# Performance work log

Hardware: AMD Instinct MI355X
Metric: run time of the kernel (lower is better)

Reference implementation:

```python
import jax, jax.numpy as jnp
import numpy as np

MODEL_DIM = 1024
NUM_HEADS = 16
HEAD_DIM = MODEL_DIM // NUM_HEADS
B, L = 2, 2048


def setup_inputs() -> dict:
    key = jax.random.key(0)
    ks = jax.random.split(key, 11)
    s = 1.0 / np.sqrt(MODEL_DIM)
    inp = {
        "q": jax.random.normal(ks[0], (B, L, MODEL_DIM), jnp.float32),
        "k": jax.random.normal(ks[1], (B, L, MODEL_DIM), jnp.float32),
        "v": jax.random.normal(ks[2], (B, L, MODEL_DIM), jnp.float32),
        "Wq": jax.random.uniform(ks[3], (MODEL_DIM, MODEL_DIM), jnp.float32, -s, s),
        "bq": jax.random.uniform(ks[4], (MODEL_DIM,), jnp.float32, -s, s),
        "Wk": jax.random.uniform(ks[5], (MODEL_DIM, MODEL_DIM), jnp.float32, -s, s),
        "bk": jax.random.uniform(ks[6], (MODEL_DIM,), jnp.float32, -s, s),
        "Wv": jax.random.uniform(ks[7], (MODEL_DIM, MODEL_DIM), jnp.float32, -s, s),
        "bv": jax.random.uniform(ks[8], (MODEL_DIM,), jnp.float32, -s, s),
        "Wo": jax.random.uniform(ks[9], (MODEL_DIM, MODEL_DIM), jnp.float32, -s, s),
        "bo": jax.random.uniform(ks[10], (MODEL_DIM,), jnp.float32, -s, s),
    }
    return inp


def reference(q, k, v, Wq, bq, Wk, bk, Wv, bv, Wo, bo):
    Bq, Lq, D = q.shape
    H, Hd = NUM_HEADS, HEAD_DIM
    # Linear projections (torch Linear: x @ W.T + b)
    Q = q @ Wq.T + bq
    K = k @ Wk.T + bk
    V = v @ Wv.T + bv
    # split heads -> [B, H, L, Hd]
    def split(x):
        return x.reshape(Bq, Lq, H, Hd).transpose(0, 2, 1, 3)
    Qh, Kh, Vh = split(Q), split(K), split(V)
    scale = 1.0 / jnp.sqrt(jnp.asarray(Hd, Q.dtype))
    scores = jnp.einsum("bhqd,bhkd->bhqk", Qh, Kh) * scale
    attn = jax.nn.softmax(scores, axis=-1)  # dropout = identity in eval
    ctx = jnp.einsum("bhqk,bhkd->bhqd", attn, Vh)
    ctx = ctx.transpose(0, 2, 1, 3).reshape(Bq, Lq, D)
    return ctx @ Wo.T + bo
```

## Files before the change

kernel.cpp:

```cpp
#include <hip/hip_runtime.h>


typedef __attribute__((ext_vector_type(4))) float f32x4;
typedef __attribute__((ext_vector_type(16))) float f32x16;
typedef __attribute__((ext_vector_type(4))) unsigned int u32x4;
typedef __attribute__((ext_vector_type(2))) unsigned int u32x2;
typedef __attribute__((ext_vector_type(8))) short bf16x8;

#define DEVI static __device__ __forceinline__

DEVI unsigned short f2bf(float x) {
  union { float f; unsigned u; } v; v.f = x;
  unsigned r = v.u + 0x7fffu + ((v.u >> 16) & 1u);
  return (unsigned short)(r >> 16);
}

DEVI unsigned cvtpk(float lo, float hi) {
  unsigned r;
  asm("v_cvt_pk_bf16_f32 %0, %1, %2" : "=v"(r) : "v"(lo), "v"(hi));
  return r;
}

DEVI float exp2v(float x) {
  float y;
  asm("v_exp_f32 %0, %1" : "=v"(y) : "v"(x));
  return y;
}

DEVI void gload_lds16(const void* g, void* l) {
  __builtin_amdgcn_global_load_lds((__attribute__((address_space(1))) void*)g,
                                   (__attribute__((address_space(3))) void*)l, 16, 0, 0);
}

#define WAIT_VM(N) asm volatile("s_waitcnt vmcnt(" #N ")" ::: "memory")
#define BARRIER __builtin_amdgcn_s_barrier()

constexpr int MD = 1024;
constexpr int NH = 16;
constexpr int HD = 64;
constexpr int LL = 2048;
constexpr float CQ = 0.18033688011112042f;

struct Cvt4Args { const float* src[4]; unsigned short* dst[4]; };

__global__ void cvt4_kernel(Cvt4Args a) {
  const int which = blockIdx.x >> 9;
  const int i = ((blockIdx.x & 511) * 256 + threadIdx.x) * 8;
  const float* w = a.src[which];
  unsigned short* o = a.dst[which];
  f32x4 x = *(const f32x4*)(w + i);
  f32x4 y = *(const f32x4*)(w + i + 4);
  union { unsigned u[4]; u32x4 q; } r;
  r.u[0] = cvtpk(x[0], x[1]); r.u[1] = cvtpk(x[2], x[3]);
  r.u[2] = cvtpk(y[0], y[1]); r.u[3] = cvtpk(y[2], y[3]);
  *(u32x4*)(o + i) = r.q;
}

struct QKVArgs {
  const float* A[3];
  const unsigned short* W[3];
  const float* bias[3];
  unsigned short* out[3];
};

__global__ __launch_bounds__(256, 2) void gemm_qkv(QKVArgs args) {
  __shared__ alignas(16) float Afl[2][128 * 32];
  __shared__ alignas(16) unsigned short Bl[2][128 * 32];

  const int tid = threadIdx.x;
  const int lane = tid & 63;
  const int wave = tid >> 6;
  const int wr = wave >> 1, wc = wave & 1;
  const int lr = lane & 15, lg = lane >> 4;

  const int logical = (int)(blockIdx.x & 7) * 96 + (int)(blockIdx.x >> 3);
  const int n0 = (logical & 7) * 128;
  const int y = logical >> 3;
  const int mode = y >> 5;
  const int m0 = (y & 31) * 128;

  const float* Af = args.A[mode];
  const unsigned short* Wb = args.W[mode];
  const float* bias = args.bias[mode];
  unsigned short* Out = args.out[mode];

  const int arow_l = lane >> 3, aslot = lane & 7;
  const int wrow_l = lane >> 2, wslot = lane & 3;

  f32x4 acc[4][4] = {};

  auto stage = [&](int b, int kt) {
    const int k0 = kt * 32;
    #pragma unroll
    for (int sh = 0; sh < 4; ++sh) {
      const int row = sh * 32 + wave * 8 + arow_l;
      const int ss = aslot ^ (row & 7);
      gload_lds16((const char*)(Af + (size_t)(m0 + row) * 1024 + k0) + ss * 16,
                  (char*)&Afl[b][0] + sh * 4096 + wave * 1024);
    }
    #pragma unroll
    for (int sh = 0; sh < 2; ++sh) {
      const int row = sh * 64 + wave * 16 + wrow_l;
      const int ss = wslot ^ ((row >> 1) & 3);
      gload_lds16((const char*)(Wb + (size_t)(n0 + row) * 1024 + k0) + ss * 16,
                  (char*)&Bl[b][0] + sh * 4096 + wave * 1024);
    }
  };

  stage(0, 0);

  for (int kt = 0; kt < 32; ++kt) {
    const int buf = kt & 1;
    if (kt < 31) {
      stage(buf ^ 1, kt + 1);
      WAIT_VM(6);
    } else {
      WAIT_VM(0);
    }
    BARRIER;

    bf16x8 af[4], bfr[4];
    #pragma unroll
    for (int mi = 0; mi < 4; ++mi) {
      const int row = wr * 64 + mi * 16 + lr;
      const char* base = (const char*)&Afl[buf][0] + row * 128;
      f32x4 a0 = *(const f32x4*)(base + ((((unsigned)lg * 2)     ^ (row & 7)) << 4));
      f32x4 a1 = *(const f32x4*)(base + ((((unsigned)lg * 2 + 1) ^ (row & 7)) << 4));
      union { unsigned u[4]; bf16x8 v; } t;
      t.u[0] = cvtpk(a0[0], a0[1]); t.u[1] = cvtpk(a0[2], a0[3]);
      t.u[2] = cvtpk(a1[0], a1[1]); t.u[3] = cvtpk(a1[2], a1[3]);
      af[mi] = t.v;
    }
    #pragma unroll
    for (int ni = 0; ni < 4; ++ni) {
      const int row = wc * 64 + ni * 16 + lr;
      bfr[ni] = *(const bf16x8*)((const char*)&Bl[buf][0] + row * 64 +
                                 (((unsigned)lg ^ ((row >> 1) & 3)) << 4));
    }

    __builtin_amdgcn_s_setprio(1);
    #pragma unroll
    for (int mi = 0; mi < 4; ++mi)
      #pragma unroll
      for (int ni = 0; ni < 4; ++ni)
        acc[mi][ni] = __builtin_amdgcn_mfma_f32_16x16x32_bf16(af[mi], bfr[ni], acc[mi][ni], 0, 0, 0);
    __builtin_amdgcn_s_setprio(0);
    BARRIER;
  }

  float bv[4];
  const int cn = n0 + wc * 64 + lr;
  #pragma unroll
  for (int ni = 0; ni < 4; ++ni) bv[ni] = bias[cn + ni * 16];

  #pragma unroll
  for (int mi = 0; mi < 4; ++mi) {
    #pragma unroll
    for (int j = 0; j < 4; ++j) {
      const int m = m0 + wr * 64 + mi * 16 + lg * 4 + j;
      const int b = m >> 11, l = m & 2047;
      #pragma unroll
      for (int ni = 0; ni < 4; ++ni) {
        const int n = cn + ni * 16;
        const int h = n >> 6, d = n & 63;
        float val = acc[mi][ni][j] + bv[ni];
        if (mode == 0) val *= CQ;
        if (mode == 2)
          Out[((size_t)(b * NH + h) * HD + d) * LL + l] = f2bf(val);
        else
          Out[((size_t)(b * NH + h) * LL + l) * HD + d] = f2bf(val);
      }
    }
  }
}

__global__ __launch_bounds__(256, 2) void gemm_out(const unsigned short* __restrict__ Ab,
                                                   const unsigned short* __restrict__ Wb,
                                                   const float* __restrict__ bias,
                                                   float* __restrict__ Out) {
  __shared__ alignas(16) unsigned short Al[2][128 * 32];
  __shared__ alignas(16) unsigned short Bl[2][128 * 32];

  const int tid = threadIdx.x;
  const int lane = tid & 63;
  const int wave = tid >> 6;
  const int wr = wave >> 1, wc = wave & 1;
  const int lr = lane & 15, lg = lane >> 4;

  const int logical = (int)(blockIdx.x & 7) * 32 + (int)(blockIdx.x >> 3);
  const int n0 = (logical & 7) * 128;
  const int m0 = (logical >> 3) * 128;

  const int wrow = tid >> 2, wslot = tid & 3;

  f32x4 acc[4][4] = {};

  auto stage = [&](int b, int kt, const unsigned short* src, unsigned short* dstbase) {
    const int k0 = kt * 32;
    #pragma unroll
    for (int shot = 0; shot < 2; ++shot) {
      const int row = shot * 64 + wrow;
      const int ss = wslot ^ ((row >> 1) & 3);
      gload_lds16((const char*)(src + (size_t)row * 1024 + k0) + ss * 16,
                  (char*)dstbase + shot * 4096 + wave * 1024);
    }
  };

  stage(0, 0, Ab + (size_t)m0 * 1024, &Al[0][0]);
  stage(0, 0, Wb + (size_t)n0 * 1024, &Bl[0][0]);

  for (int kt = 0; kt < 32; ++kt) {
    const int buf = kt & 1;
    if (kt < 31) {
      stage(buf ^ 1, kt + 1, Ab + (size_t)m0 * 1024, &Al[buf ^ 1][0]);
      stage(buf ^ 1, kt + 1, Wb + (size_t)n0 * 1024, &Bl[buf ^ 1][0]);
      WAIT_VM(4);
    } else {
      WAIT_VM(0);
    }
    BARRIER;

    bf16x8 af[4], bfr[4];
    #pragma unroll
    for (int mi = 0; mi < 4; ++mi) {
      const int row = wr * 64 + mi * 16 + lr;
      af[mi] = *(const bf16x8*)((const char*)&Al[buf][0] + row * 64 +
                                (((unsigned)lg ^ ((row >> 1) & 3)) << 4));
    }
    #pragma unroll
    for (int ni = 0; ni < 4; ++ni) {
      const int row = wc * 64 + ni * 16 + lr;
      bfr[ni] = *(const bf16x8*)((const char*)&Bl[buf][0] + row * 64 +
                                 (((unsigned)lg ^ ((row >> 1) & 3)) << 4));
    }
    __builtin_amdgcn_s_setprio(1);
    #pragma unroll
    for (int mi = 0; mi < 4; ++mi)
      #pragma unroll
      for (int ni = 0; ni < 4; ++ni)
        acc[mi][ni] = __builtin_amdgcn_mfma_f32_16x16x32_bf16(af[mi], bfr[ni], acc[mi][ni], 0, 0, 0);
    __builtin_amdgcn_s_setprio(0);
    BARRIER;
  }

  float bv[4];
  const int cn = n0 + wc * 64 + lr;
  #pragma unroll
  for (int ni = 0; ni < 4; ++ni) bv[ni] = bias[cn + ni * 16];

  #pragma unroll
  for (int mi = 0; mi < 4; ++mi)
    #pragma unroll
    for (int j = 0; j < 4; ++j) {
      const int m = m0 + wr * 64 + mi * 16 + lg * 4 + j;
      #pragma unroll
      for (int ni = 0; ni < 4; ++ni)
        Out[(size_t)m * 1024 + cn + ni * 16] = acc[mi][ni][j] + bv[ni];
    }
}

__global__ __launch_bounds__(256, 2) void attn_kernel(const unsigned short* __restrict__ Qh,
                                                      const unsigned short* __restrict__ Kh,
                                                      const unsigned short* __restrict__ Vt,
                                                      unsigned short* __restrict__ Ctx) {
  constexpr int KB = 64;
  constexpr int NT = LL / KB;
  __shared__ alignas(16) unsigned short Kl[2][KB * HD];
  __shared__ alignas(16) unsigned short Vl[2][HD * KB];

  const int tid = threadIdx.x;
  const int lane = tid & 63;
  const int wave = tid >> 6;
  const int lq = lane & 31;
  const int hi = lane >> 5;

  const int logical = (int)(blockIdx.x & 7) * 64 + (int)(blockIdx.x >> 3);
  const int bh = logical >> 4;
  const int q0 = (logical & 15) * 128 + wave * 32;

  const unsigned short* Kg = Kh + (size_t)bh * LL * HD;
  const unsigned short* Vg = Vt + (size_t)bh * HD * LL;

  bf16x8 qf[4];
  {
    const unsigned short* qp = Qh + (size_t)bh * LL * HD + (size_t)(q0 + lq) * HD + hi * 8;
    #pragma unroll
    for (int s = 0; s < 4; ++s) qf[s] = *(const bf16x8*)(qp + s * 16);
  }

  f32x16 oacc0 = {}, oacc1 = {};
  float m_ = -1e30f, s_ = 0.f;

  auto stage = [&](int b, int t) {
    #pragma unroll
    for (int shot = 0; shot < 2; ++shot) {
      const int o = shot * 4096 + tid * 16;
      const int row = o >> 7, col = o & 127;
      const int sc = col ^ ((row & 7) << 4);
      gload_lds16((const char*)Kg + (size_t)(t * KB + row) * (HD * 2) + sc,
                  (char*)&Kl[b][0] + shot * 4096 + wave * 1024);
    }
    #pragma unroll
    for (int shot = 0; shot < 2; ++shot) {
      const int o = shot * 4096 + tid * 16;
      const int row = o >> 7, col = o & 127;
      const int sc = col ^ ((row & 7) << 4);
      gload_lds16((const char*)Vg + (size_t)row * (LL * 2) + t * (KB * 2) + sc,
                  (char*)&Vl[b][0] + shot * 4096 + wave * 1024);
    }
  };

  stage(0, 0);

  for (int t = 0; t < NT; ++t) {
    const int buf = t & 1;
    if (t + 1 < NT) {
      stage(buf ^ 1, t + 1);
      WAIT_VM(4);
    } else {
      WAIT_VM(0);
    }
    BARRIER;

    f32x16 st0 = {}, st1 = {};
    const int swz = (lq & 7) << 4;
    __builtin_amdgcn_s_setprio(1);
    #pragma unroll
    for (int s = 0; s < 4; ++s) {
      const int off = ((s * 32 + hi * 16) ^ swz);
      bf16x8 k0 = *(const bf16x8*)((const char*)&Kl[buf][0] + lq * 128 + off);
      bf16x8 k1 = *(const bf16x8*)((const char*)&Kl[buf][0] + (32 + lq) * 128 + off);
      st0 = __builtin_amdgcn_mfma_f32_32x32x16_bf16(k0, qf[s], st0, 0, 0, 0);
      st1 = __builtin_amdgcn_mfma_f32_32x32x16_bf16(k1, qf[s], st1, 0, 0, 0);
    }
    __builtin_amdgcn_s_setprio(0);

    float tv[8];
    #pragma unroll
    for (int i = 0; i < 8; ++i)
      tv[i] = fmaxf(fmaxf(st0[i], st0[i + 8]), fmaxf(st1[i], st1[i + 8]));
    float pmax = fmaxf(fmaxf(fmaxf(tv[0], tv[1]), fmaxf(tv[2], tv[3])),
                       fmaxf(fmaxf(tv[4], tv[5]), fmaxf(tv[6], tv[7])));
    pmax = fmaxf(pmax, __shfl_xor(pmax, 32));

    if (!__all(pmax - m_ <= 8.f)) {
      const float nm = fmaxf(m_, pmax);
      const float al = exp2v(m_ - nm);
      m_ = nm;
      s_ *= al;
      #pragma unroll
      for (int i = 0; i < 16; ++i) { oacc0[i] *= al; oacc1[i] *= al; }
    }

    float a4[4] = {0.f, 0.f, 0.f, 0.f};
    #pragma unroll
    for (int i = 0; i < 16; ++i) {
      float y0 = exp2v(st0[i] - m_);
      float y1 = exp2v(st1[i] - m_);
      st0[i] = y0; st1[i] = y1;
      a4[i & 3] += y0; a4[i & 3] += y1;
    }
    s_ += (a4[0] + a4[1]) + (a4[2] + a4[3]);

    bf16x8 pfr[4];
    #pragma unroll
    for (int s = 0; s < 4; ++s) {
      const int r = (s & 1) * 8;
      float p0, p1, p2, p3, p4, p5, p6, p7;
      if (s < 2) {
        p0 = st0[r+0]; p1 = st0[r+1]; p2 = st0[r+2]; p3 = st0[r+3];
        p4 = st0[r+4]; p5 = st0[r+5]; p6 = st0[r+6]; p7 = st0[r+7];
      } else {
        p0 = st1[r+0]; p1 = st1[r+1]; p2 = st1[r+2]; p3 = st1[r+3];
        p4 = st1[r+4]; p5 = st1[r+5]; p6 = st1[r+6]; p7 = st1[r+7];
      }
      const unsigned A0 = cvtpk(p0, p1);
      const unsigned A1 = cvtpk(p2, p3);
      const unsigned A2 = cvtpk(p4, p5);
      const unsigned A3 = cvtpk(p6, p7);
      const unsigned t0 = (unsigned)__shfl_xor((int)A0, 32);
      const unsigned t1 = (unsigned)__shfl_xor((int)A1, 32);
      const unsigned t2 = (unsigned)__shfl_xor((int)A2, 32);
      const unsigned t3 = (unsigned)__shfl_xor((int)A3, 32);
      union { unsigned u[4]; bf16x8 v; } pf;
      pf.u[0] = hi ? t2 : A0;
      pf.u[1] = hi ? t3 : A1;
      pf.u[2] = hi ? A2 : t0;
      pf.u[3] = hi ? A3 : t1;
      pfr[s] = pf.v;
    }

    __builtin_amdgcn_s_setprio(1);
    #pragma unroll
    for (int s = 0; s < 4; ++s) {
      const int off = ((s * 32 + hi * 16) ^ swz);
      bf16x8 v0 = *(const bf16x8*)((const char*)&Vl[buf][0] + lq * 128 + off);
      bf16x8 v1 = *(const bf16x8*)((const char*)&Vl[buf][0] + (32 + lq) * 128 + off);
      oacc0 = __builtin_amdgcn_mfma_f32_32x32x16_bf16(v0, pfr[s], oacc0, 0, 0, 0);
      oacc1 = __builtin_amdgcn_mfma_f32_32x32x16_bf16(v1, pfr[s], oacc1, 0, 0, 0);
    }
    __builtin_amdgcn_s_setprio(0);
    BARRIER;
  }

  s_ += __shfl_xor(s_, 32);
  const float inv = 1.0f / s_;
  const int b = bh >> 4, h = bh & 15;
  const int q = q0 + lq;
  unsigned short* op = Ctx + ((size_t)(b * LL + q)) * MD + h * HD;
  #pragma unroll
  for (int g = 0; g < 4; ++g) {
    {
      union { unsigned short us[4]; u32x2 u; } w;
      #pragma unroll
      for (int j = 0; j < 4; ++j) w.us[j] = f2bf(oacc0[g * 4 + j] * inv);
      *(u32x2*)(op + 8 * g + 4 * hi) = w.u;
    }
    {
      union { unsigned short us[4]; u32x2 u; } w;
      #pragma unroll
      for (int j = 0; j < 4; ++j) w.us[j] = f2bf(oacc1[g * 4 + j] * inv);
      *(u32x2*)(op + 32 + 8 * g + 4 * hi) = w.u;
    }
  }
}

extern "C" void kernel_launch(void* const* d_in, const int* in_sizes, int n_in,
                              void* d_out, int out_size, void* d_ws, size_t ws_size,
                              hipStream_t stream) {
  const float* q  = (const float*)d_in[0];
  const float* k  = (const float*)d_in[1];
  const float* v  = (const float*)d_in[2];
  const float* Wq = (const float*)d_in[3];
  const float* bq = (const float*)d_in[4];
  const float* Wk = (const float*)d_in[5];
  const float* bk = (const float*)d_in[6];
  const float* Wv = (const float*)d_in[7];
  const float* bv = (const float*)d_in[8];
  const float* Wo = (const float*)d_in[9];
  const float* bo = (const float*)d_in[10];

  char* ws = (char*)d_ws;
  const size_t MB = 1u << 20;
  unsigned short* Wqb = (unsigned short*)(ws + 0 * MB);
  unsigned short* Wkb = (unsigned short*)(ws + 2 * MB);
  unsigned short* Wvb = (unsigned short*)(ws + 4 * MB);
  unsigned short* Wob = (unsigned short*)(ws + 6 * MB);
  unsigned short* Qhb = (unsigned short*)(ws + 8 * MB);
  unsigned short* Khb = (unsigned short*)(ws + 16 * MB);
  unsigned short* Vtb = (unsigned short*)(ws + 24 * MB);
  unsigned short* ctx = (unsigned short*)(ws + 32 * MB);

  Cvt4Args ca;
  ca.src[0] = Wq; ca.src[1] = Wk; ca.src[2] = Wv; ca.src[3] = Wo;
  ca.dst[0] = Wqb; ca.dst[1] = Wkb; ca.dst[2] = Wvb; ca.dst[3] = Wob;
  cvt4_kernel<<<2048, 256, 0, stream>>>(ca);

  QKVArgs args;
  args.A[0] = q;  args.A[1] = k;  args.A[2] = v;
  args.W[0] = Wqb; args.W[1] = Wkb; args.W[2] = Wvb;
  args.bias[0] = bq; args.bias[1] = bk; args.bias[2] = bv;
  args.out[0] = Qhb; args.out[1] = Khb; args.out[2] = Vtb;
  gemm_qkv<<<768, 256, 0, stream>>>(args);

  attn_kernel<<<512, 256, 0, stream>>>(Qhb, Khb, Vtb, ctx);

  gemm_out<<<256, 256, 0, stream>>>(ctx, Wob, bo, (float*)d_out);
}
```

Before: 146.0 us.

## Pre-convert activations to bf16 and deepen LDS pipelines to four stages

Extends the conversion kernel so the q/k/v activations are also converted to bf16 ahead of time. The QKV GEMM then loads bf16 A tiles directly instead of loading fp32 and converting them in the inner loop. All three main kernels (QKV GEMM, attention, output GEMM) move from double-buffered to four-slot LDS ring buffers with three tiles prefetched, so more loads are in flight. The trade-offs are an extra round trip of the activations through memory, a larger conversion launch, and more LDS per block, which may reduce occupancy.

```diff
diff --git a/kernel.cpp b/kernel.cpp
--- a/kernel.cpp
+++ b/kernel.cpp
@@ -41,13 +41,16 @@
 constexpr int LL = 2048;
 constexpr float CQ = 0.18033688011112042f;
 
-struct Cvt4Args { const float* src[4]; unsigned short* dst[4]; };
-
-__global__ void cvt4_kernel(Cvt4Args a) {
-  const int which = blockIdx.x >> 9;
-  const int i = ((blockIdx.x & 511) * 256 + threadIdx.x) * 8;
+struct CvtArgs { const float* src[7]; unsigned short* dst[7]; };
+
+__global__ void cvt_kernel(CvtArgs a) {
+  const int bx = blockIdx.x;
+  int which, base;
+  if (bx < 2048) { which = bx >> 9;            base = (bx & 511) * 2048; }
+  else           { which = 4 + ((bx - 2048) >> 11); base = ((bx - 2048) & 2047) * 2048; }
   const float* w = a.src[which];
   unsigned short* o = a.dst[which];
+  const int i = base + threadIdx.x * 8;
   f32x4 x = *(const f32x4*)(w + i);
   f32x4 y = *(const f32x4*)(w + i + 4);
   union { unsigned u[4]; u32x4 q; } r;
@@ -57,15 +60,15 @@
 }
 
 struct QKVArgs {
-  const float* A[3];
+  const unsigned short* A[3];
   const unsigned short* W[3];
   const float* bias[3];
   unsigned short* out[3];
 };
 
 __global__ __launch_bounds__(256, 2) void gemm_qkv(QKVArgs args) {
-  __shared__ alignas(16) float Afl[2][128 * 32];
-  __shared__ alignas(16) unsigned short Bl[2][128 * 32];
+  __shared__ alignas(16) unsigned short Abuf[4][128 * 32];
+  __shared__ alignas(16) unsigned short Bbuf[4][128 * 32];
 
   const int tid = threadIdx.x;
   const int lane = tid & 63;
@@ -79,62 +82,54 @@
   const int mode = y >> 5;
   const int m0 = (y & 31) * 128;
 
-  const float* Af = args.A[mode];
+  const unsigned short* Ab = args.A[mode];
   const unsigned short* Wb = args.W[mode];
   const float* bias = args.bias[mode];
   unsigned short* Out = args.out[mode];
 
-  const int arow_l = lane >> 3, aslot = lane & 7;
-  const int wrow_l = lane >> 2, wslot = lane & 3;
+  const int rrow = lane >> 2, rslot = lane & 3;
 
   f32x4 acc[4][4] = {};
 
-  auto stage = [&](int b, int kt) {
+  auto stage = [&](int slot, int kt) {
     const int k0 = kt * 32;
     #pragma unroll
-    for (int sh = 0; sh < 4; ++sh) {
-      const int row = sh * 32 + wave * 8 + arow_l;
-      const int ss = aslot ^ (row & 7);
-      gload_lds16((const char*)(Af + (size_t)(m0 + row) * 1024 + k0) + ss * 16,
-                  (char*)&Afl[b][0] + sh * 4096 + wave * 1024);
-    }
-    #pragma unroll
     for (int sh = 0; sh < 2; ++sh) {
-      const int row = sh * 64 + wave * 16 + wrow_l;
-      const int ss = wslot ^ ((row >> 1) & 3);
+      const int row = sh * 64 + wave * 16 + rrow;
+      const int ss = rslot ^ ((row >> 1) & 3);
+      gload_lds16((const char*)(Ab + (size_t)(m0 + row) * 1024 + k0) + ss * 16,
+                  (char*)&Abuf[slot][0] + sh * 4096 + wave * 1024);
+    }
+    #pragma unroll
+    for (int sh = 0; sh < 2; ++sh) {
+      const int row = sh * 64 + wave * 16 + rrow;
+      const int ss = rslot ^ ((row >> 1) & 3);
       gload_lds16((const char*)(Wb + (size_t)(n0 + row) * 1024 + k0) + ss * 16,
-                  (char*)&Bl[b][0] + sh * 4096 + wave * 1024);
+                  (char*)&Bbuf[slot][0] + sh * 4096 + wave * 1024);
     }
   };
 
-  stage(0, 0);
+  stage(0, 0); stage(1, 1); stage(2, 2);
 
   for (int kt = 0; kt < 32; ++kt) {
-    const int buf = kt & 1;
-    if (kt < 31) {
-      stage(buf ^ 1, kt + 1);
-      WAIT_VM(6);
-    } else {
-      WAIT_VM(0);
-    }
+    const int slot = kt & 3;
+    if (kt < 29)      { stage((kt + 3) & 3, kt + 3); WAIT_VM(12); }
+    else if (kt == 29) WAIT_VM(8);
+    else if (kt == 30) WAIT_VM(4);
+    else               WAIT_VM(0);
     BARRIER;
 
     bf16x8 af[4], bfr[4];
     #pragma unroll
     for (int mi = 0; mi < 4; ++mi) {
       const int row = wr * 64 + mi * 16 + lr;
-      const char* base = (const char*)&Afl[buf][0] + row * 128;
-      f32x4 a0 = *(const f32x4*)(base + ((((unsigned)lg * 2)     ^ (row & 7)) << 4));
-      f32x4 a1 = *(const f32x4*)(base + ((((unsigned)lg * 2 + 1) ^ (row & 7)) << 4));
-      union { unsigned u[4]; bf16x8 v; } t;
-      t.u[0] = cvtpk(a0[0], a0[1]); t.u[1] = cvtpk(a0[2], a0[3]);
-      t.u[2] = cvtpk(a1[0], a1[1]); t.u[3] = cvtpk(a1[2], a1[3]);
-      af[mi] = t.v;
+      af[mi] = *(const bf16x8*)((const char*)&Abuf[slot][0] + row * 64 +
+                                (((unsigned)lg ^ ((row >> 1) & 3)) << 4));
     }
     #pragma unroll
     for (int ni = 0; ni < 4; ++ni) {
       const int row = wc * 64 + ni * 16 + lr;
-      bfr[ni] = *(const bf16x8*)((const char*)&Bl[buf][0] + row * 64 +
+      bfr[ni] = *(const bf16x8*)((const char*)&Bbuf[slot][0] + row * 64 +
                                  (((unsigned)lg ^ ((row >> 1) & 3)) << 4));
     }
 
@@ -178,8 +173,8 @@
                                                    const unsigned short* __restrict__ Wb,
                                                    const float* __restrict__ bias,
                                                    float* __restrict__ Out) {
-  __shared__ alignas(16) unsigned short Al[2][128 * 32];
-  __shared__ alignas(16) unsigned short Bl[2][128 * 32];
+  __shared__ alignas(16) unsigned short Abuf[4][128 * 32];
+  __shared__ alignas(16) unsigned short Bbuf[4][128 * 32];
 
   const int tid = threadIdx.x;
   const int lane = tid & 63;
@@ -191,46 +186,49 @@
   const int n0 = (logical & 7) * 128;
   const int m0 = (logical >> 3) * 128;
 
-  const int wrow = tid >> 2, wslot = tid & 3;
+  const int rrow = lane >> 2, rslot = lane & 3;
 
   f32x4 acc[4][4] = {};
 
-  auto stage = [&](int b, int kt, const unsigned short* src, unsigned short* dstbase) {
+  auto stage = [&](int slot, int kt) {
     const int k0 = kt * 32;
     #pragma unroll
-    for (int shot = 0; shot < 2; ++shot) {
-      const int row = shot * 64 + wrow;
-      const int ss = wslot ^ ((row >> 1) & 3);
-      gload_lds16((const char*)(src + (size_t)row * 1024 + k0) + ss * 16,
-                  (char*)dstbase + shot * 4096 + wave * 1024);
+    for (int sh = 0; sh < 2; ++sh) {
+      const int row = sh * 64 + wave * 16 + rrow;
+      const int ss = rslot ^ ((row >> 1) & 3);
+      gload_lds16((const char*)(Ab + (size_t)(m0 + row) * 1024 + k0) + ss * 16,
+                  (char*)&Abuf[slot][0] + sh * 4096 + wave * 1024);
+    }
+    #pragma unroll
+    for (int sh = 0; sh < 2; ++sh) {
+      const int row = sh * 64 + wave * 16 + rrow;
+      const int ss = rslot ^ ((row >> 1) & 3);
+      gload_lds16((const char*)(Wb + (size_t)(n0 + row) * 1024 + k0) + ss * 16,
+                  (char*)&Bbuf[slot][0] + sh * 4096 + wave * 1024);
     }
   };
 
-  stage(0, 0, Ab + (size_t)m0 * 1024, &Al[0][0]);
-  stage(0, 0, Wb + (size_t)n0 * 1024, &Bl[0][0]);
+  stage(0, 0); stage(1, 1); stage(2, 2);
 
   for (int kt = 0; kt < 32; ++kt) {
-    const int buf = kt & 1;
-    if (kt < 31) {
-      stage(buf ^ 1, kt + 1, Ab + (size_t)m0 * 1024, &Al[buf ^ 1][0]);
-      stage(buf ^ 1, kt + 1, Wb + (size_t)n0 * 1024, &Bl[buf ^ 1][0]);
-      WAIT_VM(4);
-    } else {
-      WAIT_VM(0);
-    }
+    const int slot = kt & 3;
+    if (kt < 29)      { stage((kt + 3) & 3, kt + 3); WAIT_VM(12); }
+    else if (kt == 29) WAIT_VM(8);
+    else if (kt == 30) WAIT_VM(4);
+    else               WAIT_VM(0);
     BARRIER;
 
     bf16x8 af[4], bfr[4];
     #pragma unroll
     for (int mi = 0; mi < 4; ++mi) {
       const int row = wr * 64 + mi * 16 + lr;
-      af[mi] = *(const bf16x8*)((const char*)&Al[buf][0] + row * 64 +
+      af[mi] = *(const bf16x8*)((const char*)&Abuf[slot][0] + row * 64 +
                                 (((unsigned)lg ^ ((row >> 1) & 3)) << 4));
     }
     #pragma unroll
     for (int ni = 0; ni < 4; ++ni) {
       const int row = wc * 64 + ni * 16 + lr;
-      bfr[ni] = *(const bf16x8*)((const char*)&Bl[buf][0] + row * 64 +
+      bfr[ni] = *(const bf16x8*)((const char*)&Bbuf[slot][0] + row * 64 +
                                  (((unsigned)lg ^ ((row >> 1) & 3)) << 4));
     }
     __builtin_amdgcn_s_setprio(1);
@@ -265,8 +263,8 @@
                                                       unsigned short* __restrict__ Ctx) {
   constexpr int KB = 64;
   constexpr int NT = LL / KB;
-  __shared__ alignas(16) unsigned short Kl[2][KB * HD];
-  __shared__ alignas(16) unsigned short Vl[2][HD * KB];
+  __shared__ alignas(16) unsigned short Kl[4][KB * HD];
+  __shared__ alignas(16) unsigned short Vl[4][HD * KB];
 
   const int tid = threadIdx.x;
   const int lane = tid & 63;
@@ -291,14 +289,14 @@
   f32x16 oacc0 = {}, oacc1 = {};
   float m_ = -1e30f, s_ = 0.f;
 
-  auto stage = [&](int b, int t) {
+  auto stage = [&](int slot, int t) {
     #pragma unroll
     for (int shot = 0; shot < 2; ++shot) {
       const int o = shot * 4096 + tid * 16;
       const int row = o >> 7, col = o & 127;
       const int sc = col ^ ((row & 7) << 4);
       gload_lds16((const char*)Kg + (size_t)(t * KB + row) * (HD * 2) + sc,
-                  (char*)&Kl[b][0] + shot * 4096 + wave * 1024);
+                  (char*)&Kl[slot][0] + shot * 4096 + wave * 1024);
     }
     #pragma unroll
     for (int shot = 0; shot < 2; ++shot) {
@@ -306,20 +304,18 @@
       const int row = o >> 7, col = o & 127;
       const int sc = col ^ ((row & 7) << 4);
       gload_lds16((const char*)Vg + (size_t)row * (LL * 2) + t * (KB * 2) + sc,
-                  (char*)&Vl[b][0] + shot * 4096 + wave * 1024);
+                  (char*)&Vl[slot][0] + shot * 4096 + wave * 1024);
     }
   };
 
-  stage(0, 0);
+  stage(0, 0); stage(1, 1); stage(2, 2);
 
   for (int t = 0; t < NT; ++t) {
-    const int buf = t & 1;
-    if (t + 1 < NT) {
-      stage(buf ^ 1, t + 1);
-      WAIT_VM(4);
-    } else {
-      WAIT_VM(0);
-    }
+    const int slot = t & 3;
+    if (t < 29)      { stage((t + 3) & 3, t + 3); WAIT_VM(12); }
+    else if (t == 29) WAIT_VM(8);
+    else if (t == 30) WAIT_VM(4);
+    else              WAIT_VM(0);
     BARRIER;
 
     f32x16 st0 = {}, st1 = {};
@@ -328,8 +324,8 @@
     #pragma unroll
     for (int s = 0; s < 4; ++s) {
       const int off = ((s * 32 + hi * 16) ^ swz);
-      bf16x8 k0 = *(const bf16x8*)((const char*)&Kl[buf][0] + lq * 128 + off);
-      bf16x8 k1 = *(const bf16x8*)((const char*)&Kl[buf][0] + (32 + lq) * 128 + off);
+      bf16x8 k0 = *(const bf16x8*)((const char*)&Kl[slot][0] + lq * 128 + off);
+      bf16x8 k1 = *(const bf16x8*)((const char*)&Kl[slot][0] + (32 + lq) * 128 + off);
       st0 = __builtin_amdgcn_mfma_f32_32x32x16_bf16(k0, qf[s], st0, 0, 0, 0);
       st1 = __builtin_amdgcn_mfma_f32_32x32x16_bf16(k1, qf[s], st1, 0, 0, 0);
     }
@@ -394,8 +390,8 @@
     #pragma unroll
     for (int s = 0; s < 4; ++s) {
       const int off = ((s * 32 + hi * 16) ^ swz);
-      bf16x8 v0 = *(const bf16x8*)((const char*)&Vl[buf][0] + lq * 128 + off);
-      bf16x8 v1 = *(const bf16x8*)((const char*)&Vl[buf][0] + (32 + lq) * 128 + off);
+      bf16x8 v0 = *(const bf16x8*)((const char*)&Vl[slot][0] + lq * 128 + off);
+      bf16x8 v1 = *(const bf16x8*)((const char*)&Vl[slot][0] + (32 + lq) * 128 + off);
       oacc0 = __builtin_amdgcn_mfma_f32_32x32x16_bf16(v0, pfr[s], oacc0, 0, 0, 0);
       oacc1 = __builtin_amdgcn_mfma_f32_32x32x16_bf16(v1, pfr[s], oacc1, 0, 0, 0);
     }
@@ -450,14 +446,19 @@
   unsigned short* Khb = (unsigned short*)(ws + 16 * MB);
   unsigned short* Vtb = (unsigned short*)(ws + 24 * MB);
   unsigned short* ctx = (unsigned short*)(ws + 32 * MB);
-
-  Cvt4Args ca;
+  unsigned short* qb  = (unsigned short*)(ws + 40 * MB);
+  unsigned short* kb  = (unsigned short*)(ws + 48 * MB);
+  unsigned short* vb  = (unsigned short*)(ws + 56 * MB);
+
+  CvtArgs ca;
   ca.src[0] = Wq; ca.src[1] = Wk; ca.src[2] = Wv; ca.src[3] = Wo;
+  ca.src[4] = q;  ca.src[5] = k;  ca.src[6] = v;
   ca.dst[0] = Wqb; ca.dst[1] = Wkb; ca.dst[2] = Wvb; ca.dst[3] = Wob;
-  cvt4_kernel<<<2048, 256, 0, stream>>>(ca);
+  ca.dst[4] = qb;  ca.dst[5] = kb;  ca.dst[6] = vb;
+  cvt_kernel<<<8192, 256, 0, stream>>>(ca);
 
   QKVArgs args;
-  args.A[0] = q;  args.A[1] = k;  args.A[2] = v;
+  args.A[0] = qb;  args.A[1] = kb;  args.A[2] = vb;
   args.W[0] = Wqb; args.W[1] = Wkb; args.W[2] = Wvb;
   args.bias[0] = bq; args.bias[1] = bk; args.bias[2] = bv;
   args.out[0] = Qhb; args.out[1] = Khb; args.out[2] = Vtb;
```

Measured after the change: 161.4 us. 10.6% more time.
